# Performance work log

Measured on AMD Instinct MI355X. Metric: run time of the kernel, lower is better.

## Reference

```python
import jax, jax.numpy as jnp
import numpy as np

NUM_CLASSES = 14
IGNORE = 0
MAX_SAMPLES = 28 * 50
MAX_VIEWS = 50
TEMP = 0.1
THRESH = 0.3


def setup_inputs() -> dict:
    key = jax.random.key(0)
    B, Fd, D, H, W = 2, 128, 16, 128, 128
    N = B * D * H * W
    feats = jax.random.normal(key, (B, Fd, D, H, W), jnp.float32)
    idx = np.arange(N)
    pred = (idx % NUM_CLASSES).astype(np.int32)
    # alternate blocks: easy (label==pred) / hard (label!=pred) so every class
    # has >max_views pixels with >= n_view/2 hard and easy samples
    block = (idx // NUM_CLASSES) % 2
    lab = np.where(block == 0, pred, (pred + 1) % NUM_CLASSES).astype(np.int32)
    labels = jnp.asarray(lab.reshape(B, D, H, W))
    predict = jnp.asarray(pred.reshape(B, D, H, W))
    probability = jnp.ones((B, D, H, W), jnp.float32)
    queue = jax.random.normal(jax.random.fold_in(key, 1), (NUM_CLASSES, 4096, Fd), jnp.float32)
    return {"feats": feats, "labels": labels, "predict": predict,
            "probability": probability, "queue": queue}


def _l2n(x):
    return x / jnp.linalg.norm(x, axis=-1, keepdims=True)


def reference(feats, labels, predict, probability, queue):
    Fd = feats.shape[1]
    # [B, Fd, D, H, W] -> [N, Fd]
    f = jnp.transpose(feats, (0, 2, 3, 4, 1)).reshape(-1, Fd)
    lab = labels.reshape(-1)
    pred = predict.reshape(-1)
    valid = probability.reshape(-1) > THRESH
    N = f.shape[0]

    total_classes = NUM_CLASSES - 1              # all non-ignore classes qualify by construction
    n_view = min(MAX_SAMPLES // total_classes, MAX_VIEWS)  # = 50
    n_hard = n_view // 2                          # balanced branch always taken
    n_easy = n_view - n_hard
    idxs = jnp.arange(N)

    def pick(mask, k):
        # deterministic stand-in for randperm: first k valid indices
        keys = jnp.where(mask, idxs, N)
        return jnp.sort(keys)[:k]

    def sample_class(c):
        hard = valid & (pred == c) & (lab != c)
        easy = valid & (pred == c) & (lab == c)
        sel = jnp.concatenate([pick(hard, n_hard), pick(easy, n_easy)])
        return f[sel]

    classes = jnp.arange(1, NUM_CLASSES)
    X_ = jax.vmap(sample_class)(classes)          # [C-1, n_view, Fd]

    # positive queue: per-class mean of (threshold-filtered) feats
    onehot = jax.nn.one_hot(lab, NUM_CLASSES, dtype=f.dtype) * valid[:, None].astype(f.dtype)
    sums = jnp.einsum('nc,nd->cd', onehot, f)     # [C, Fd]
    cnts = onehot.sum(0)[:, None]
    pos_queue = sums / cnts                        # [C, Fd]

    # negatives: second half of cache, classes 1..C-1 (class 0 skipped in _sample_negative)
    neg = queue[1:, queue.shape[1] // 2:, :]       # [C-1, M, Fd]

    a = _l2n(X_)                                   # [C-1, V, Fd]
    p = _l2n(pos_queue[1:])                        # [C-1, Fd]
    n = _l2n(neg)                                  # [C-1, M, Fd]

    logits = jnp.einsum('cvd,cd->cv', a, p) / TEMP           # [C-1, V]
    neg_sum = jnp.exp(jnp.einsum('cvd,cmd->cvm', a, n) / TEMP).sum(-1)  # [C-1, V]
    log_prob = -logits + jnp.log(jnp.exp(logits) + neg_sum)
    # sum over classes of per-class mean, divided by num classes
    return log_prob.mean(axis=1).mean()
```

## Files before the change

kernel.cpp:

```cpp
#include <hip/hip_runtime.h>

#define NUMC 14
#define FD 128
#define SPATIAL (16*128*128)
#define N_TOTAL (2*SPATIAL)
#define NV 50
#define NH 25
#define TC 13
#define QLEN 4096
#define MCH 64
#define NCHUNK 32
#define CHUNK 1024
#define NBLKP (N_TOTAL / CHUNK)
#define PXB 32768
#define CHB (SPATIAL / PXB)
#define NSUMBLK (256 * CHB)
#define THRESH_F 0.3f
#define RSTR 35

#define WS_SEL     0
#define WS_ANORM   656
#define WS_CNTS    1312
#define WS_SUMS    1328
#define WS_NEGPART 3120
#define WS_AROWS   23920
#define WS_PART    107120
#define WS_CNTPART 135792
#define WS_LAB8    143984

__global__ void k_select(const int* __restrict__ labels, const int* __restrict__ predict,
                         const float* __restrict__ prob, int* __restrict__ sel) {
    int cat = blockIdx.x;
    int c = 1 + (cat >> 1);
    bool hard = (cat & 1) == 0;
    int lane = threadIdx.x;
    int* slot = sel + (c - 1) * NV + (hard ? 0 : NH);
    int found = 0;
    for (int base = 0; base < N_TOTAL && found < NH; base += 64) {
        int n = base + lane;
        bool m = false;
        if (n < N_TOTAL) {
            int pr = predict[n];
            if (pr == c && prob[n] > THRESH_F) {
                int lb = labels[n];
                m = hard ? (lb != c) : (lb == c);
            }
        }
        unsigned long long mask = __ballot(m);
        int rank = __popcll(mask & ((1ull << lane) - 1ull));
        if (m && (found + rank) < NH) slot[found + rank] = n;
        found += __popcll(mask);
    }
    if (lane >= found && lane < NH) slot[lane] = N_TOTAL - 1;
}

__global__ __launch_bounds__(256) void k_prep(const int* __restrict__ labels,
        const float* __restrict__ prob, unsigned char* __restrict__ lab8,
        int* __restrict__ cntpart) {
    __shared__ int cnt_s[16];
    int tid = threadIdx.x;
    int lane = tid & 63;
    int base = blockIdx.x * CHUNK;
    if (tid < 16) cnt_s[tid] = 0;
    __syncthreads();
    int n = base + tid * 4;
    int4   lb = *(const int4*)(labels + n);
    float4 pv = *(const float4*)(prob + n);
    int l0 = pv.x > THRESH_F ? (lb.x & 15) : 15;
    int l1 = pv.y > THRESH_F ? (lb.y & 15) : 15;
    int l2 = pv.z > THRESH_F ? (lb.z & 15) : 15;
    int l3 = pv.w > THRESH_F ? (lb.w & 15) : 15;
    uchar4 o;
    o.x = (unsigned char)l0; o.y = (unsigned char)l1;
    o.z = (unsigned char)l2; o.w = (unsigned char)l3;
    *(uchar4*)(lab8 + n) = o;
    #pragma unroll
    for (int c = 0; c < 16; ++c) {
        if (c == 14) continue;
        int cnt = __popcll(__ballot(l0 == c)) + __popcll(__ballot(l1 == c))
                + __popcll(__ballot(l2 == c)) + __popcll(__ballot(l3 == c));
        if (lane == 0 && cnt) atomicAdd(&cnt_s[c], cnt);
    }
    __syncthreads();
    if (tid < 16) cntpart[blockIdx.x * 16 + tid] = cnt_s[tid];
}

__global__ __launch_bounds__(256) void k_sums(const float* __restrict__ feats,
        const unsigned char* __restrict__ lab8, float* __restrict__ part) {
    __shared__ float acc_s[256 * RSTR];
    int tid = threadIdx.x;
    int plane = blockIdx.x >> 3;
    int chunk = blockIdx.x & (CHB - 1);
    int b = plane >> 7;
    for (int i = tid; i < 256 * RSTR; i += 256) acc_s[i] = 0.f;
    __syncthreads();
    const float* fp = feats + (size_t)plane * SPATIAL + chunk * PXB;
    const unsigned char* lp = lab8 + (size_t)b * SPATIAL + chunk * PXB;
    int r0 = tid * RSTR;
    int r1 = r0 + 18;
    float4 v = *(const float4*)(fp + tid * 4);
    uchar4 l = *(const uchar4*)(lp + tid * 4);
    for (int i = 0; i < PXB / 1024; ++i) {
        int ip = (i + 1 < PXB / 1024) ? i + 1 : i;
        int offn = ip * 1024 + tid * 4;
        float4 vn = *(const float4*)(fp + offn);
        uchar4 ln = *(const uchar4*)(lp + offn);
        acc_s[r0 + (l.x & 15)] += v.x;
        acc_s[r1 + (l.y & 15)] += v.y;
        acc_s[r0 + (l.z & 15)] += v.z;
        acc_s[r1 + (l.w & 15)] += v.w;
        v = vn; l = ln;
    }
    __syncthreads();
    #pragma unroll
    for (int c = 0; c < NUMC; ++c) acc_s[r0 + c] += acc_s[r1 + c];
    __syncthreads();
    for (int s = 128; s >= 16; s >>= 1) {
        if (tid < s) {
            #pragma unroll
            for (int c = 0; c < NUMC; ++c)
                acc_s[tid * RSTR + c] += acc_s[(tid + s) * RSTR + c];
        }
        __syncthreads();
    }
    if (tid < NUMC) {
        float s = 0.f;
        #pragma unroll
        for (int r = 0; r < 16; ++r) s += acc_s[r * RSTR + tid];
        part[blockIdx.x * NUMC + tid] = s;
    }
}

__global__ __launch_bounds__(256) void k_reduce(const float* __restrict__ part,
        const int* __restrict__ cntpart, float* __restrict__ sums, float* __restrict__ cnts) {
    int idx = blockIdx.x * 256 + threadIdx.x;
    if (idx < NUMC * FD) {
        int c = idx >> 7, ch = idx & 127;
        float s = 0.f;
        #pragma unroll
        for (int b = 0; b < 2; ++b)
            #pragma unroll
            for (int k = 0; k < CHB; ++k)
                s += part[(size_t)(((b << 7) + ch) * CHB + k) * NUMC + c];
        sums[idx] = s;
    } else if (idx < NUMC * FD + 16) {
        int j = idx - NUMC * FD;
        int s = 0;
        for (int b = 0; b < NBLKP; ++b) s += cntpart[b * 16 + j];
        cnts[j] = (float)s;
    }
}

__global__ __launch_bounds__(128) void k_gather(const float* __restrict__ feats,
        const int* __restrict__ sel, float* __restrict__ arows, float* __restrict__ anorm) {
    __shared__ float red[2];
    int r = blockIdx.x;
    int t = threadIdx.x;
    int n = sel[r];
    int b = n >> 18, sp = n & (SPATIAL - 1);
    float v = feats[((size_t)(b * FD + t)) * SPATIAL + sp];
    arows[r * FD + t] = v;
    float a = v * v;
    #pragma unroll
    for (int o = 32; o; o >>= 1) a += __shfl_xor(a, o);
    if ((t & 63) == 0) red[t >> 6] = a;
    __syncthreads();
    if (t == 0) anorm[r] = sqrtf(red[0] + red[1]);
}

__global__ __launch_bounds__(256) void k_neg(const float* __restrict__ queue,
        const float* __restrict__ arows, const float* __restrict__ anorm,
        float* __restrict__ negpart) {
    constexpr int NSTR = FD + 4;
    __shared__ float a_s[NV * FD];
    __shared__ float n_s[MCH * NSTR];
    __shared__ float an_s[NV];
    int tid = threadIdx.x;
    int ci = blockIdx.x >> 5;
    int chunk = blockIdx.x & 31;
    const float* ap = arows + ci * (NV * FD);
    for (int i = tid; i < NV * FD / 4; i += 256) ((float4*)a_s)[i] = ((const float4*)ap)[i];
    if (tid < NV) an_s[tid] = anorm[ci * NV + tid];
    const float* qp = queue + ((size_t)(ci + 1) * QLEN + (QLEN / 2) + chunk * MCH) * (size_t)FD;
    for (int i = tid; i < MCH * FD / 4; i += 256) {
        int m = i / (FD / 4), k4 = i % (FD / 4);
        ((float4*)(n_s + m * NSTR))[k4] = ((const float4*)qp)[i];
    }
    __syncthreads();
    int lane = tid & 63, w = tid >> 6;
    float4 nr[FD / 4];
    const float4* nrow = (const float4*)(n_s + lane * NSTR);
    float sq = 0.f;
    #pragma unroll
    for (int k = 0; k < FD / 4; ++k) {
        nr[k] = nrow[k];
        sq += nr[k].x*nr[k].x + nr[k].y*nr[k].y + nr[k].z*nr[k].z + nr[k].w*nr[k].w;
    }
    float inn = 10.f / sqrtf(sq);
    float* np = negpart + chunk * (TC * NV) + ci * NV;
    for (int v = w; v < NV; v += 4) {
        const float4* a4 = (const float4*)(a_s + v * FD);
        float dot = 0.f;
        #pragma unroll
        for (int k = 0; k < FD / 4; ++k) {
            float4 x = a4[k];
            dot += x.x*nr[k].x + x.y*nr[k].y + x.z*nr[k].z + x.w*nr[k].w;
        }
        float e = __expf(dot * inn / an_s[v]);
        #pragma unroll
        for (int o = 32; o; o >>= 1) e += __shfl_xor(e, o);
        if (lane == 0) np[v] = e;
    }
}

__global__ __launch_bounds__(256) void k_final(const float* __restrict__ arows,
        const float* __restrict__ anorm, const float* __restrict__ sums,
        const float* __restrict__ cnts, const float* __restrict__ negpart,
        float* __restrict__ out) {
    __shared__ float p_s[TC * FD];
    __shared__ float pn_s[TC];
    __shared__ float red[256];
    int tid = threadIdx.x;
    for (int i = tid; i < TC * FD; i += 256) {
        int c = i >> 7, k = i & 127;
        p_s[i] = sums[(c + 1) * FD + k] / cnts[c + 1];
    }
    __syncthreads();
    if (tid < TC) {
        float s = 0.f;
        for (int k = 0; k < FD; ++k) { float v = p_s[tid * FD + k]; s += v * v; }
        pn_s[tid] = sqrtf(s);
    }
    __syncthreads();
    float acc = 0.f;
    for (int r = tid; r < TC * NV; r += 256) {
        int c = r / NV;
        const float4* ar4 = (const float4*)(arows + r * FD);
        const float4* p4  = (const float4*)(p_s + c * FD);
        float dot = 0.f;
        #pragma unroll
        for (int k = 0; k < FD / 4; ++k) {
            float4 x = ar4[k], y = p4[k];
            dot += x.x*y.x + x.y*y.y + x.z*y.z + x.w*y.w;
        }
        float logit = dot / (anorm[r] * pn_s[c] * 0.1f);
        float ns = 0.f;
        for (int ch = 0; ch < NCHUNK; ++ch) ns += negpart[ch * (TC * NV) + r];
        acc += -logit + logf(__expf(logit) + ns);
    }
    red[tid] = acc;
    __syncthreads();
    for (int s = 128; s; s >>= 1) {
        if (tid < s) red[tid] += red[tid + s];
        __syncthreads();
    }
    if (tid == 0) out[0] = red[0] * (1.f / (TC * NV));
}

extern "C" void kernel_launch(void* const* d_in, const int* in_sizes, int n_in,
                              void* d_out, int out_size, void* d_ws, size_t ws_size,
                              hipStream_t stream) {
    (void)in_sizes; (void)n_in; (void)out_size; (void)ws_size;
    const float* feats   = (const float*)d_in[0];
    const int*   labels  = (const int*)d_in[1];
    const int*   predict = (const int*)d_in[2];
    const float* prob    = (const float*)d_in[3];
    const float* queue   = (const float*)d_in[4];
    float* ws  = (float*)d_ws;
    float* out = (float*)d_out;

    int*   sel     = (int*)(ws + WS_SEL);
    float* anorm   = ws + WS_ANORM;
    float* cnts    = ws + WS_CNTS;
    float* sums    = ws + WS_SUMS;
    float* negpart = ws + WS_NEGPART;
    float* arows   = ws + WS_AROWS;
    float* part    = ws + WS_PART;
    int*   cntpart = (int*)(ws + WS_CNTPART);
    unsigned char* lab8 = (unsigned char*)(ws + WS_LAB8);

    k_select <<<26, 64, 0, stream>>>(labels, predict, prob, sel);
    k_prep   <<<NBLKP, 256, 0, stream>>>(labels, prob, lab8, cntpart);
    k_sums   <<<NSUMBLK, 256, 0, stream>>>(feats, lab8, part);
    k_reduce <<<8, 256, 0, stream>>>(part, cntpart, sums, cnts);
    k_gather <<<TC * NV, 128, 0, stream>>>(feats, sel, arows, anorm);
    k_neg    <<<TC * NCHUNK, 256, 0, stream>>>(queue, arows, anorm, negpart);
    k_final  <<<1, 256, 0, stream>>>(arows, anorm, sums, cnts, negpart, out);
}
```

Baseline: 113.4 us.

## Register-accumulate class sums over channel groups; split final reduction across classes

New measurement: 132.3 us. +16.7%, slower.

```diff
diff --git a/kernel.cpp b/kernel.cpp
--- a/kernel.cpp
+++ b/kernel.cpp
@@ -12,11 +12,15 @@
 #define NCHUNK 32
 #define CHUNK 1024
 #define NBLKP (N_TOTAL / CHUNK)
-#define PXB 32768
-#define CHB (SPATIAL / PXB)
-#define NSUMBLK (256 * CHB)
 #define THRESH_F 0.3f
-#define RSTR 35
+
+#define CGRP 8
+#define NCG (FD / CGRP)
+#define PPT 64
+#define PXBLK (256 * PPT)
+#define NPB (N_TOTAL / PXBLK)
+#define NSUMBLK (NCG * NPB)
+#define PARTW (NUMC * CGRP)
 
 #define WS_SEL     0
 #define WS_ANORM   656
@@ -24,9 +28,10 @@
 #define WS_SUMS    1328
 #define WS_NEGPART 3120
 #define WS_AROWS   23920
-#define WS_PART    107120
-#define WS_CNTPART 135792
-#define WS_LAB8    143984
+#define WS_LOSSP   107120
+#define WS_PART    107200
+#define WS_CNTPART 336576
+#define WS_LAB8    344768
 
 __global__ void k_select(const int* __restrict__ labels, const int* __restrict__ predict,
                          const float* __restrict__ prob, int* __restrict__ sel) {
@@ -87,61 +92,61 @@
 
 __global__ __launch_bounds__(256) void k_sums(const float* __restrict__ feats,
         const unsigned char* __restrict__ lab8, float* __restrict__ part) {
-    __shared__ float acc_s[256 * RSTR];
-    int tid = threadIdx.x;
-    int plane = blockIdx.x >> 3;
-    int chunk = blockIdx.x & (CHB - 1);
-    int b = plane >> 7;
-    for (int i = tid; i < 256 * RSTR; i += 256) acc_s[i] = 0.f;
-    __syncthreads();
-    const float* fp = feats + (size_t)plane * SPATIAL + chunk * PXB;
-    const unsigned char* lp = lab8 + (size_t)b * SPATIAL + chunk * PXB;
-    int r0 = tid * RSTR;
-    int r1 = r0 + 18;
-    float4 v = *(const float4*)(fp + tid * 4);
-    uchar4 l = *(const uchar4*)(lp + tid * 4);
-    for (int i = 0; i < PXB / 1024; ++i) {
-        int ip = (i + 1 < PXB / 1024) ? i + 1 : i;
-        int offn = ip * 1024 + tid * 4;
-        float4 vn = *(const float4*)(fp + offn);
-        uchar4 ln = *(const uchar4*)(lp + offn);
-        acc_s[r0 + (l.x & 15)] += v.x;
-        acc_s[r1 + (l.y & 15)] += v.y;
-        acc_s[r0 + (l.z & 15)] += v.z;
-        acc_s[r1 + (l.w & 15)] += v.w;
-        v = vn; l = ln;
-    }
-    __syncthreads();
-    #pragma unroll
-    for (int c = 0; c < NUMC; ++c) acc_s[r0 + c] += acc_s[r1 + c];
-    __syncthreads();
-    for (int s = 128; s >= 16; s >>= 1) {
-        if (tid < s) {
+    int tid = threadIdx.x;
+    int g  = blockIdx.x >> 5;
+    int pb = blockIdx.x & 31;
+    int px0 = pb * PXBLK;
+    int b   = px0 >> 18;
+    int sp0 = px0 & (SPATIAL - 1);
+    const float* fp = feats + (size_t)(b * FD + g * CGRP) * SPATIAL + sp0;
+    const unsigned char* lp = lab8 + (size_t)b * SPATIAL + sp0;
+
+    float acc[NUMC][CGRP];
+    #pragma unroll
+    for (int c = 0; c < NUMC; ++c)
+        #pragma unroll
+        for (int j = 0; j < CGRP; ++j) acc[c][j] = 0.f;
+
+    #pragma unroll 2
+    for (int i = 0; i < PPT; ++i) {
+        int off = (i << 8) + tid;
+        int l = lp[off];
+        float v[CGRP];
+        #pragma unroll
+        for (int j = 0; j < CGRP; ++j)
+            v[j] = __builtin_nontemporal_load(fp + (size_t)j * SPATIAL + off);
+        float m[NUMC];
+        #pragma unroll
+        for (int c = 0; c < NUMC; ++c) m[c] = (l == c) ? 1.f : 0.f;
+        #pragma unroll
+        for (int c = 0; c < NUMC; ++c)
             #pragma unroll
-            for (int c = 0; c < NUMC; ++c)
-                acc_s[tid * RSTR + c] += acc_s[(tid + s) * RSTR + c];
+            for (int j = 0; j < CGRP; ++j)
+                acc[c][j] = fmaf(m[c], v[j], acc[c][j]);
+    }
+
+    int lane = tid & 63, w = tid >> 6;
+    float* pw = part + ((size_t)blockIdx.x * 4 + w) * PARTW;
+    #pragma unroll
+    for (int c = 0; c < NUMC; ++c)
+        #pragma unroll
+        for (int j = 0; j < CGRP; ++j) {
+            float x = acc[c][j];
+            #pragma unroll
+            for (int o = 32; o; o >>= 1) x += __shfl_xor(x, o);
+            if (lane == 0) pw[c * CGRP + j] = x;
         }
-        __syncthreads();
-    }
-    if (tid < NUMC) {
-        float s = 0.f;
-        #pragma unroll
-        for (int r = 0; r < 16; ++r) s += acc_s[r * RSTR + tid];
-        part[blockIdx.x * NUMC + tid] = s;
-    }
 }
 
 __global__ __launch_bounds__(256) void k_reduce(const float* __restrict__ part,
         const int* __restrict__ cntpart, float* __restrict__ sums, float* __restrict__ cnts) {
     int idx = blockIdx.x * 256 + threadIdx.x;
     if (idx < NUMC * FD) {
-        int c = idx >> 7, ch = idx & 127;
+        int cls = idx >> 7, ch = idx & 127;
+        int g = ch >> 3, cj = ch & 7;
+        const float* pp = part + (size_t)g * (32 * 4 * PARTW) + cls * CGRP + cj;
         float s = 0.f;
-        #pragma unroll
-        for (int b = 0; b < 2; ++b)
-            #pragma unroll
-            for (int k = 0; k < CHB; ++k)
-                s += part[(size_t)(((b << 7) + ch) * CHB + k) * NUMC + c];
+        for (int t = 0; t < 128; ++t) s += pp[(size_t)t * PARTW];
         sums[idx] = s;
     } else if (idx < NUMC * FD + 16) {
         int j = idx - NUMC * FD;
@@ -197,7 +202,7 @@
         sq += nr[k].x*nr[k].x + nr[k].y*nr[k].y + nr[k].z*nr[k].z + nr[k].w*nr[k].w;
     }
     float inn = 10.f / sqrtf(sq);
-    float* np = negpart + chunk * (TC * NV) + ci * NV;
+    float* np = negpart + (ci * NV) * NCHUNK + chunk;
     for (int v = w; v < NV; v += 4) {
         const float4* a4 = (const float4*)(a_s + v * FD);
         float dot = 0.f;
@@ -209,52 +214,60 @@
         float e = __expf(dot * inn / an_s[v]);
         #pragma unroll
         for (int o = 32; o; o >>= 1) e += __shfl_xor(e, o);
-        if (lane == 0) np[v] = e;
-    }
-}
-
-__global__ __launch_bounds__(256) void k_final(const float* __restrict__ arows,
+        if (lane == 0) np[v * NCHUNK] = e;
+    }
+}
+
+__global__ __launch_bounds__(256) void k_final_a(const float* __restrict__ arows,
         const float* __restrict__ anorm, const float* __restrict__ sums,
         const float* __restrict__ cnts, const float* __restrict__ negpart,
-        float* __restrict__ out) {
-    __shared__ float p_s[TC * FD];
-    __shared__ float pn_s[TC];
-    __shared__ float red[256];
-    int tid = threadIdx.x;
-    for (int i = tid; i < TC * FD; i += 256) {
-        int c = i >> 7, k = i & 127;
-        p_s[i] = sums[(c + 1) * FD + k] / cnts[c + 1];
-    }
-    __syncthreads();
-    if (tid < TC) {
+        float* __restrict__ lossp) {
+    __shared__ float p_s[FD];
+    __shared__ float red_s[2];
+    __shared__ float lacc[8];
+    int tid = threadIdx.x;
+    int ci = blockIdx.x, c = ci + 1;
+    if (tid < 128) p_s[tid] = sums[c * FD + tid] / cnts[c];
+    __syncthreads();
+    if (tid < 128) {
+        float q = p_s[tid] * p_s[tid];
+        #pragma unroll
+        for (int o = 32; o; o >>= 1) q += __shfl_xor(q, o);
+        if ((tid & 63) == 0) red_s[tid >> 6] = q;
+    }
+    __syncthreads();
+    float inv10 = 10.f / sqrtf(red_s[0] + red_s[1]);
+    int grp = tid >> 5, l32 = tid & 31;
+    float acc = 0.f;
+    for (int r = grp; r < NV; r += 8) {
+        int ar = ci * NV + r;
+        float4 x = ((const float4*)arows)[ar * 32 + l32];
+        float4 y = ((const float4*)p_s)[l32];
+        float d = x.x*y.x + x.y*y.y + x.z*y.z + x.w*y.w;
+        float ns = negpart[ar * 32 + l32];
+        #pragma unroll
+        for (int o = 16; o; o >>= 1) { d += __shfl_xor(d, o); ns += __shfl_xor(ns, o); }
+        if (l32 == 0) {
+            float logit = d * inv10 / anorm[ar];
+            acc += -logit + logf(__expf(logit) + ns);
+        }
+    }
+    if (l32 == 0) lacc[grp] = acc;
+    __syncthreads();
+    if (tid == 0) {
         float s = 0.f;
-        for (int k = 0; k < FD; ++k) { float v = p_s[tid * FD + k]; s += v * v; }
-        pn_s[tid] = sqrtf(s);
-    }
-    __syncthreads();
-    float acc = 0.f;
-    for (int r = tid; r < TC * NV; r += 256) {
-        int c = r / NV;
-        const float4* ar4 = (const float4*)(arows + r * FD);
-        const float4* p4  = (const float4*)(p_s + c * FD);
-        float dot = 0.f;
-        #pragma unroll
-        for (int k = 0; k < FD / 4; ++k) {
-            float4 x = ar4[k], y = p4[k];
-            dot += x.x*y.x + x.y*y.y + x.z*y.z + x.w*y.w;
-        }
-        float logit = dot / (anorm[r] * pn_s[c] * 0.1f);
-        float ns = 0.f;
-        for (int ch = 0; ch < NCHUNK; ++ch) ns += negpart[ch * (TC * NV) + r];
-        acc += -logit + logf(__expf(logit) + ns);
-    }
-    red[tid] = acc;
-    __syncthreads();
-    for (int s = 128; s; s >>= 1) {
-        if (tid < s) red[tid] += red[tid + s];
-        __syncthreads();
-    }
-    if (tid == 0) out[0] = red[0] * (1.f / (TC * NV));
+        #pragma unroll
+        for (int i = 0; i < 8; ++i) s += lacc[i];
+        lossp[ci] = s;
+    }
+}
+
+__global__ void k_final_b(const float* __restrict__ lossp, float* __restrict__ out) {
+    int tid = threadIdx.x;
+    float v = (tid < TC) ? lossp[tid] : 0.f;
+    #pragma unroll
+    for (int o = 32; o; o >>= 1) v += __shfl_xor(v, o);
+    if (tid == 0) out[0] = v * (1.f / (TC * NV));
 }
 
 extern "C" void kernel_launch(void* const* d_in, const int* in_sizes, int n_in,
@@ -275,6 +288,7 @@
     float* sums    = ws + WS_SUMS;
     float* negpart = ws + WS_NEGPART;
     float* arows   = ws + WS_AROWS;
+    float* lossp   = ws + WS_LOSSP;
     float* part    = ws + WS_PART;
     int*   cntpart = (int*)(ws + WS_CNTPART);
     unsigned char* lab8 = (unsigned char*)(ws + WS_LAB8);
@@ -285,5 +299,6 @@
     k_reduce <<<8, 256, 0, stream>>>(part, cntpart, sums, cnts);
     k_gather <<<TC * NV, 128, 0, stream>>>(feats, sel, arows, anorm);
     k_neg    <<<TC * NCHUNK, 256, 0, stream>>>(queue, arows, anorm, negpart);
-    k_final  <<<1, 256, 0, stream>>>(arows, anorm, sums, cnts, negpart, out);
-}
+    k_final_a<<<TC, 256, 0, stream>>>(arows, anorm, sums, cnts, negpart, lossp);
+    k_final_b<<<1, 64, 0, stream>>>(lossp, out);
+}
```
